# Optimization experiments

Hardware: AMD Instinct MI355X
Metric: run time of the kernel (lower is better)

## Reference

```python
import jax, jax.numpy as jnp
import numpy as np

NUM_USERS = 80000
NUM_ITEMS = 40000
N_NODES = NUM_USERS + NUM_ITEMS
EMB = 128
NNZ = 600000
BATCH = 4096
N_LAYERS = 3


def setup_inputs() -> dict:
    key = jax.random.key(0)
    ks = jax.random.split(key, 8)
    users = jax.random.randint(ks[0], (BATCH,), 0, NUM_USERS)
    pos_items = jax.random.randint(ks[1], (BATCH,), 0, NUM_ITEMS)
    neg_items = jax.random.randint(ks[2], (BATCH,), 0, NUM_ITEMS)
    user_emb = jax.random.normal(ks[3], (NUM_USERS, EMB), dtype=jnp.float32)
    item_emb = jax.random.normal(ks[4], (NUM_ITEMS, EMB), dtype=jnp.float32)
    adj_row = jax.random.randint(ks[5], (NNZ,), 0, N_NODES)
    adj_col = jax.random.randint(ks[6], (NNZ,), 0, N_NODES)
    adj_val = jax.random.uniform(ks[7], (NNZ,), dtype=jnp.float32)
    return {
        "users": users, "pos_items": pos_items, "neg_items": neg_items,
        "user_emb": user_emb, "item_emb": item_emb,
        "adj_row": adj_row, "adj_col": adj_col, "adj_val": adj_val,
        "n_layers": N_LAYERS,
    }


def _spmm(row, col, val, x, n_nodes):
    # sparse (COO) adjacency @ dense x : [N, D]
    return jax.ops.segment_sum(val[:, None] * x[col], row, num_segments=n_nodes)


def reference(users, pos_items, neg_items, user_emb, item_emb, adj_row, adj_col, adj_val, n_layers):
    num_users = user_emb.shape[0]
    n_nodes = num_users + item_emb.shape[0]
    ego = jnp.concatenate([user_emb, item_emb], axis=0)  # [N, D]
    acc = ego
    h = ego
    for _ in range(n_layers):
        h = _spmm(adj_row, adj_col, adj_val, h, n_nodes)
        acc = acc + h
    final = acc / jnp.asarray(n_layers + 1, dtype=acc.dtype)  # mean over layer stack
    u_g = final[:num_users]
    i_g = final[num_users:]
    return (u_g[users], i_g[pos_items], i_g[neg_items], i_g)
```

## Files before the change

kernel.cpp:

```cpp
#include <hip/hip_runtime.h>
#include <hip/hip_fp16.h>

#define EMB      128
#define NUSERS   80000
#define NITEMS   40000
#define NNODES   120000
#define NNZV     600000
#define BATCHN   4096
#define WELL     24

typedef unsigned int u32;

__device__ __forceinline__ u32 pack2(float lo, float hi) {
    u32 a = __float_as_uint(lo), b = __float_as_uint(hi);
    a = (a + 0x7FFFu + ((a >> 16) & 1u)) >> 16;
    b = (b + 0x7FFFu + ((b >> 16) & 1u)) >> 16;
    return a | (b << 16);
}
__device__ __forceinline__ float lo2f(u32 u) { return __uint_as_float(u << 16); }
__device__ __forceinline__ float hi2f(u32 u) { return __uint_as_float(u & 0xFFFF0000u); }

__device__ __forceinline__ float val15(u32 w) {
    return __half2float(__ushort_as_half((unsigned short)(w & 0x7FFFu)));
}

#define CVT_N (NNODES * EMB / 8)
__global__ __launch_bounds__(256) void convert_ego(
    const float* __restrict__ ue, const float* __restrict__ ie,
    u32* __restrict__ ego)
{
    int t = blockIdx.x * 256 + threadIdx.x;
    if (t >= CVT_N) return;
    const float4* s = (t < NUSERS * EMB / 8)
        ? ((const float4*)ue) + (size_t)t * 2
        : ((const float4*)ie) + ((size_t)t - NUSERS * EMB / 8) * 2;
    float4 a = s[0], b = s[1];
    uint4 o;
    o.x = pack2(a.x, a.y); o.y = pack2(a.z, a.w);
    o.z = pack2(b.x, b.y); o.w = pack2(b.z, b.w);
    ((uint4*)ego)[t] = o;
}

__global__ __launch_bounds__(256) void build_ell(
    const int* __restrict__ row, const int* __restrict__ col,
    const float* __restrict__ val,
    int* __restrict__ counts, u32* __restrict__ ell)
{
    int e = blockIdx.x * 256 + threadIdx.x;
    if (e >= NNZV) return;
    int r = row[e];
    int s = atomicAdd(&counts[r], 1);
    if (s < WELL) {
        u32 entry = ((u32)col[e] << 15)
                  | (u32)__half_as_ushort(__float2half_rn(val[e]));
        ell[(size_t)r * WELL + s] = entry;
    }
}

__device__ __forceinline__ void gath8(
    const u32* __restrict__ src, const u32* __restrict__ e, u32 voff,
    float& a0, float& a1)
{
    u32 w0 = e[0], w1 = e[1], w2 = e[2], w3 = e[3];
    u32 w4 = e[4], w5 = e[5], w6 = e[6], w7 = e[7];
    const u32* p0 = src + ((size_t)(w0 >> 15) << 6);
    const u32* p1 = src + ((size_t)(w1 >> 15) << 6);
    const u32* p2 = src + ((size_t)(w2 >> 15) << 6);
    const u32* p3 = src + ((size_t)(w3 >> 15) << 6);
    const u32* p4 = src + ((size_t)(w4 >> 15) << 6);
    const u32* p5 = src + ((size_t)(w5 >> 15) << 6);
    const u32* p6 = src + ((size_t)(w6 >> 15) << 6);
    const u32* p7 = src + ((size_t)(w7 >> 15) << 6);
    u32 x0, x1, x2, x3, x4, x5, x6, x7;
    asm volatile(
        "global_load_dword %[x0], %[v], %[s0]\n\t"
        "global_load_dword %[x1], %[v], %[s1]\n\t"
        "global_load_dword %[x2], %[v], %[s2]\n\t"
        "global_load_dword %[x3], %[v], %[s3]\n\t"
        "global_load_dword %[x4], %[v], %[s4]\n\t"
        "global_load_dword %[x5], %[v], %[s5]\n\t"
        "global_load_dword %[x6], %[v], %[s6]\n\t"
        "global_load_dword %[x7], %[v], %[s7]\n\t"
        "s_waitcnt vmcnt(0)"
        : [x0]"=&v"(x0), [x1]"=&v"(x1), [x2]"=&v"(x2), [x3]"=&v"(x3),
          [x4]"=&v"(x4), [x5]"=&v"(x5), [x6]"=&v"(x6), [x7]"=&v"(x7)
        : [v]"v"(voff),
          [s0]"s"(p0), [s1]"s"(p1), [s2]"s"(p2), [s3]"s"(p3),
          [s4]"s"(p4), [s5]"s"(p5), [s6]"s"(p6), [s7]"s"(p7)
        : "memory");
    float v0 = val15(w0), v1 = val15(w1), v2 = val15(w2), v3 = val15(w3);
    float v4 = val15(w4), v5 = val15(w5), v6 = val15(w6), v7 = val15(w7);
    a0 += v0*lo2f(x0) + v1*lo2f(x1) + v2*lo2f(x2) + v3*lo2f(x3)
        + v4*lo2f(x4) + v5*lo2f(x5) + v6*lo2f(x6) + v7*lo2f(x7);
    a1 += v0*hi2f(x0) + v1*hi2f(x1) + v2*hi2f(x2) + v3*hi2f(x3)
        + v4*hi2f(x4) + v5*hi2f(x5) + v6*hi2f(x6) + v7*hi2f(x7);
}

__device__ __forceinline__ float2 row_accum(
    int r, u32 voff, const int* __restrict__ counts,
    const u32* __restrict__ ell, const u32* __restrict__ src)
{
    const u32* e = ell + (size_t)r * WELL;
    int c = counts[r];
    float a0 = 0.f, a1 = 0.f;
    gath8(src, e, voff, a0, a1);
    if (c > 8) {
        gath8(src, e + 8, voff, a0, a1);
        if (c > 16)
            gath8(src, e + 16, voff, a0, a1);
    }
    return make_float2(a0, a1);
}

__global__ __launch_bounds__(256) void spmm_ell(
    const int* __restrict__ counts, const u32* __restrict__ ell,
    const u32* __restrict__ src, u32* __restrict__ dst)
{
    int wid = (blockIdx.x * 256 + threadIdx.x) >> 6;
    int r = __builtin_amdgcn_readfirstlane(wid);
    int lane = threadIdx.x & 63;
    float2 a = row_accum(r, lane * 4, counts, ell, src);
    dst[((size_t)r << 6) + lane] = pack2(a.x, a.y);
}

__global__ __launch_bounds__(256) void spmm3_finalize(
    const int* __restrict__ users,
    const int* __restrict__ counts, const u32* __restrict__ ell,
    const float* __restrict__ ue, const float* __restrict__ ie,
    const u32* __restrict__ h1, const u32* __restrict__ h2,
    float* __restrict__ out)
{
    int wid = (blockIdx.x * 256 + threadIdx.x) >> 6;
    int w = __builtin_amdgcn_readfirstlane(wid);
    int lane = threadIdx.x & 63;
    int r = (w < BATCHN) ? users[w] : NUSERS + (w - BATCHN);
    float2 a = row_accum(r, lane * 4, counts, ell, h2);
    const float2* eg = (r < NUSERS)
        ? (const float2*)(ue + (size_t)r * EMB)
        : (const float2*)(ie + (size_t)(r - NUSERS) * EMB);
    float2 g = eg[lane];
    u32 b1 = h1[((size_t)r << 6) + lane];
    u32 b2 = h2[((size_t)r << 6) + lane];
    float2 o;
    o.x = (g.x + lo2f(b1) + lo2f(b2) + a.x) * 0.25f;
    o.y = (g.y + hi2f(b1) + hi2f(b2) + a.y) * 0.25f;
    float2* dst = (w < BATCHN)
        ? (float2*)out + (size_t)w * 64
        : (float2*)(out + (size_t)3 * BATCHN * EMB) + (size_t)(w - BATCHN) * 64;
    dst[lane] = o;
}

__global__ __launch_bounds__(256) void gather_pn(
    const int* __restrict__ pos, const int* __restrict__ neg,
    const float* __restrict__ ig, float* __restrict__ out)
{
    int b = blockIdx.x * 8 + (threadIdx.x >> 5);
    int lane = threadIdx.x & 31;
    int idx = (b < BATCHN) ? pos[b] : neg[b - BATCHN];
    float4 x = ((const float4*)(ig + (size_t)idx * EMB))[lane];
    ((float4*)(out + (size_t)(BATCHN + b) * EMB))[lane] = x;
}

extern "C" void kernel_launch(void* const* d_in, const int* in_sizes, int n_in,
                              void* d_out, int out_size, void* d_ws, size_t ws_size,
                              hipStream_t stream)
{
    const int*   users = (const int*)d_in[0];
    const int*   pos   = (const int*)d_in[1];
    const int*   neg   = (const int*)d_in[2];
    const float* ue    = (const float*)d_in[3];
    const float* ie    = (const float*)d_in[4];
    const int*   arow  = (const int*)d_in[5];
    const int*   acol  = (const int*)d_in[6];
    const float* aval  = (const float*)d_in[7];

    const size_t hU = (size_t)NNODES * 64;
    char* ws = (char*)d_ws;
    u32* h2     = (u32*)ws;  ws += hU * sizeof(u32);
    u32* h1     = (u32*)ws;  ws += hU * sizeof(u32);
    u32* ego    = (u32*)ws;  ws += hU * sizeof(u32);
    u32* ell    = (u32*)ws;  ws += (size_t)NNODES * WELL * sizeof(u32);
    int* counts = (int*)ws;  ws += NNODES * sizeof(int);

    hipMemsetAsync(ell, 0,
        (size_t)NNODES * WELL * sizeof(u32) + NNODES * sizeof(int), stream);

    convert_ego<<<CVT_N / 256 + 1, 256, 0, stream>>>(ue, ie, ego);

    int eblk256 = (NNZV + 255) / 256;
    build_ell<<<eblk256, 256, 0, stream>>>(arow, acol, aval, counts, ell);

    spmm_ell<<<NNODES / 4, 256, 0, stream>>>(counts, ell, ego, h1);
    spmm_ell<<<NNODES / 4, 256, 0, stream>>>(counts, ell, h1, h2);

    float* out = (float*)d_out;
    spmm3_finalize<<<(BATCHN + NITEMS) / 4, 256, 0, stream>>>(
        users, counts, ell, ue, ie, h1, h2, out);

    float* ig = out + (size_t)3 * BATCHN * EMB;
    gather_pn<<<(2 * BATCHN) / 8, 256, 0, stream>>>(pos, neg, ig, out);
}
```

Before: 132.7 us.

## Drop ELL memset, pad atomic counters, and mask unused ELL slots

Removes the memset of the whole ELL table plus counts. Unfilled ELL slots are instead made harmless by clamping column indices and zeroing weights for slots past the row count. The counters are spread to one per 64-byte stride so the atomics in build_ell hit different cache lines, and they are zeroed inside the convert kernel. The cost is a 16x larger counter array to zero, extra min/select work in the gather, and loads of stale slots that may fetch rows which are then multiplied by zero.

Measured after the change: 128.4 us. 3.2% less time.

```diff
diff --git a/kernel.cpp b/kernel.cpp
--- a/kernel.cpp
+++ b/kernel.cpp
@@ -8,6 +8,7 @@
 #define NNZV     600000
 #define BATCHN   4096
 #define WELL     24
+#define CSTR     16
 
 typedef unsigned int u32;
 
@@ -24,21 +25,26 @@
     return __half2float(__ushort_as_half((unsigned short)(w & 0x7FFFu)));
 }
 
-#define CVT_N (NNODES * EMB / 8)
+#define CVT_N  (NNODES * EMB / 8)
+#define FILL_N (NNODES * CSTR / 4)
 __global__ __launch_bounds__(256) void convert_ego(
     const float* __restrict__ ue, const float* __restrict__ ie,
-    u32* __restrict__ ego)
+    u32* __restrict__ ego, uint4* __restrict__ counts4)
 {
     int t = blockIdx.x * 256 + threadIdx.x;
-    if (t >= CVT_N) return;
-    const float4* s = (t < NUSERS * EMB / 8)
-        ? ((const float4*)ue) + (size_t)t * 2
-        : ((const float4*)ie) + ((size_t)t - NUSERS * EMB / 8) * 2;
-    float4 a = s[0], b = s[1];
-    uint4 o;
-    o.x = pack2(a.x, a.y); o.y = pack2(a.z, a.w);
-    o.z = pack2(b.x, b.y); o.w = pack2(b.z, b.w);
-    ((uint4*)ego)[t] = o;
+    if (t < CVT_N) {
+        const float4* s = (t < NUSERS * EMB / 8)
+            ? ((const float4*)ue) + (size_t)t * 2
+            : ((const float4*)ie) + ((size_t)t - NUSERS * EMB / 8) * 2;
+        float4 a = s[0], b = s[1];
+        uint4 o;
+        o.x = pack2(a.x, a.y); o.y = pack2(a.z, a.w);
+        o.z = pack2(b.x, b.y); o.w = pack2(b.z, b.w);
+        ((uint4*)ego)[t] = o;
+    } else {
+        int f = t - CVT_N;
+        if (f < FILL_N) counts4[f] = make_uint4(0, 0, 0, 0);
+    }
 }
 
 __global__ __launch_bounds__(256) void build_ell(
@@ -49,7 +55,7 @@
     int e = blockIdx.x * 256 + threadIdx.x;
     if (e >= NNZV) return;
     int r = row[e];
-    int s = atomicAdd(&counts[r], 1);
+    int s = atomicAdd(&counts[(size_t)r << 4], 1);
     if (s < WELL) {
         u32 entry = ((u32)col[e] << 15)
                   | (u32)__half_as_ushort(__float2half_rn(val[e]));
@@ -59,18 +65,18 @@
 
 __device__ __forceinline__ void gath8(
     const u32* __restrict__ src, const u32* __restrict__ e, u32 voff,
-    float& a0, float& a1)
+    int k0, int c, float& a0, float& a1)
 {
     u32 w0 = e[0], w1 = e[1], w2 = e[2], w3 = e[3];
     u32 w4 = e[4], w5 = e[5], w6 = e[6], w7 = e[7];
-    const u32* p0 = src + ((size_t)(w0 >> 15) << 6);
-    const u32* p1 = src + ((size_t)(w1 >> 15) << 6);
-    const u32* p2 = src + ((size_t)(w2 >> 15) << 6);
-    const u32* p3 = src + ((size_t)(w3 >> 15) << 6);
-    const u32* p4 = src + ((size_t)(w4 >> 15) << 6);
-    const u32* p5 = src + ((size_t)(w5 >> 15) << 6);
-    const u32* p6 = src + ((size_t)(w6 >> 15) << 6);
-    const u32* p7 = src + ((size_t)(w7 >> 15) << 6);
+    const u32* p0 = src + ((size_t)min(w0 >> 15, NNODES - 1u) << 6);
+    const u32* p1 = src + ((size_t)min(w1 >> 15, NNODES - 1u) << 6);
+    const u32* p2 = src + ((size_t)min(w2 >> 15, NNODES - 1u) << 6);
+    const u32* p3 = src + ((size_t)min(w3 >> 15, NNODES - 1u) << 6);
+    const u32* p4 = src + ((size_t)min(w4 >> 15, NNODES - 1u) << 6);
+    const u32* p5 = src + ((size_t)min(w5 >> 15, NNODES - 1u) << 6);
+    const u32* p6 = src + ((size_t)min(w6 >> 15, NNODES - 1u) << 6);
+    const u32* p7 = src + ((size_t)min(w7 >> 15, NNODES - 1u) << 6);
     u32 x0, x1, x2, x3, x4, x5, x6, x7;
     asm volatile(
         "global_load_dword %[x0], %[v], %[s0]\n\t"
@@ -88,8 +94,14 @@
           [s0]"s"(p0), [s1]"s"(p1), [s2]"s"(p2), [s3]"s"(p3),
           [s4]"s"(p4), [s5]"s"(p5), [s6]"s"(p6), [s7]"s"(p7)
         : "memory");
-    float v0 = val15(w0), v1 = val15(w1), v2 = val15(w2), v3 = val15(w3);
-    float v4 = val15(w4), v5 = val15(w5), v6 = val15(w6), v7 = val15(w7);
+    float v0 = (k0 + 0 < c) ? val15(w0) : 0.f;
+    float v1 = (k0 + 1 < c) ? val15(w1) : 0.f;
+    float v2 = (k0 + 2 < c) ? val15(w2) : 0.f;
+    float v3 = (k0 + 3 < c) ? val15(w3) : 0.f;
+    float v4 = (k0 + 4 < c) ? val15(w4) : 0.f;
+    float v5 = (k0 + 5 < c) ? val15(w5) : 0.f;
+    float v6 = (k0 + 6 < c) ? val15(w6) : 0.f;
+    float v7 = (k0 + 7 < c) ? val15(w7) : 0.f;
     a0 += v0*lo2f(x0) + v1*lo2f(x1) + v2*lo2f(x2) + v3*lo2f(x3)
         + v4*lo2f(x4) + v5*lo2f(x5) + v6*lo2f(x6) + v7*lo2f(x7);
     a1 += v0*hi2f(x0) + v1*hi2f(x1) + v2*hi2f(x2) + v3*hi2f(x3)
@@ -101,13 +113,13 @@
     const u32* __restrict__ ell, const u32* __restrict__ src)
 {
     const u32* e = ell + (size_t)r * WELL;
-    int c = counts[r];
+    int c = min(counts[(size_t)r << 4], WELL);
     float a0 = 0.f, a1 = 0.f;
-    gath8(src, e, voff, a0, a1);
+    gath8(src, e, voff, 0, c, a0, a1);
     if (c > 8) {
-        gath8(src, e + 8, voff, a0, a1);
+        gath8(src, e + 8, voff, 8, c, a0, a1);
         if (c > 16)
-            gath8(src, e + 16, voff, a0, a1);
+            gath8(src, e + 16, voff, 16, c, a0, a1);
     }
     return make_float2(a0, a1);
 }
@@ -180,12 +192,10 @@
     u32* h1     = (u32*)ws;  ws += hU * sizeof(u32);
     u32* ego    = (u32*)ws;  ws += hU * sizeof(u32);
     u32* ell    = (u32*)ws;  ws += (size_t)NNODES * WELL * sizeof(u32);
-    int* counts = (int*)ws;  ws += NNODES * sizeof(int);
-
-    hipMemsetAsync(ell, 0,
-        (size_t)NNODES * WELL * sizeof(u32) + NNODES * sizeof(int), stream);
-
-    convert_ego<<<CVT_N / 256 + 1, 256, 0, stream>>>(ue, ie, ego);
+    int* counts = (int*)ws;  ws += (size_t)NNODES * CSTR * sizeof(int);
+
+    int cvblocks = (CVT_N + FILL_N + 255) / 256;
+    convert_ego<<<cvblocks, 256, 0, stream>>>(ue, ie, ego, (uint4*)counts);
 
     int eblk256 = (NNZV + 255) / 256;
     build_ell<<<eblk256, 256, 0, stream>>>(arow, acol, aval, counts, ell);
```
